# Performance work log

Measured on AMD Instinct MI355X. Metric: run time of the kernel, lower is better.

The kernel has to match this reference:

```python
import jax, jax.numpy as jnp
import numpy as np

DIM = 1024
HEADS = 16
DIM_HEAD = 64
INNER = HEADS * DIM_HEAD  # 1024
SCALE = DIM_HEAD ** -0.5


def setup_inputs() -> dict:
    key = jax.random.key(0)
    ks = jax.random.split(key, 5)
    B, N = 4, 2048
    x = jax.random.normal(ks[0], (B, N, DIM), dtype=jnp.float32)
    # torch Linear weights are [out, in]; store transposed [in, out] for x @ W
    s = 1.0 / np.sqrt(DIM)
    Wq = jax.random.uniform(ks[1], (DIM, INNER), minval=-s, maxval=s, dtype=jnp.float32)
    Wkv = jax.random.uniform(ks[2], (DIM, 2 * INNER), minval=-s, maxval=s, dtype=jnp.float32)
    so = 1.0 / np.sqrt(INNER)
    Wo = jax.random.uniform(ks[3], (INNER, DIM), minval=-so, maxval=so, dtype=jnp.float32)
    bo = jax.random.uniform(ks[4], (DIM,), minval=-so, maxval=so, dtype=jnp.float32)
    return {"x": x, "Wq": Wq, "Wkv": Wkv, "Wo": Wo, "bo": bo}


def reference(x, Wq, Wkv, Wo, bo):
    B, N, _ = x.shape
    q = x @ Wq                      # [B, N, INNER]
    kv = x @ Wkv                    # [B, N, 2*INNER]
    k, v = jnp.split(kv, 2, axis=-1)

    def split_heads(t):
        return t.reshape(B, N, HEADS, DIM_HEAD).transpose(0, 2, 1, 3)  # [B,H,N,D]

    q, k, v = split_heads(q) * SCALE, split_heads(k), split_heads(v)
    sim = jnp.einsum('bhid,bhjd->bhij', q, k)  # [B,H,N,N]
    mask_value = -jnp.finfo(sim.dtype).max
    # causal: mask strictly-upper triangle (triu with offset j-i+1 = 1)
    causal_mask = jnp.triu(jnp.ones((N, N), dtype=bool), k=1)
    sim = jnp.where(causal_mask[None, None, :, :], mask_value, sim)
    attn = jax.nn.softmax(sim, axis=-1)
    out = jnp.einsum('bhij,bhjd->bhid', attn, v)            # [B,H,N,D]
    out = out.transpose(0, 2, 1, 3).reshape(B, N, INNER)    # [B,N,INNER]
    return out @ Wo + bo
```

## Files before the change

kernel.cpp:

```cpp
#include <hip/hip_runtime.h>

typedef unsigned short u16;
typedef __bf16 bf16x8 __attribute__((ext_vector_type(8)));
typedef float floatx4 __attribute__((ext_vector_type(4)));
typedef unsigned as1_u32 __attribute__((address_space(1)));
typedef unsigned as3_u32 __attribute__((address_space(3)));

__device__ inline u16 f2bf(float f) {
    unsigned int u = __builtin_bit_cast(unsigned int, f);
    u += 0x7fffu + ((u >> 16) & 1u);
    return (u16)(u >> 16);
}
__device__ inline u16 f2bf_trunc(float f) {
    return (u16)(__builtin_bit_cast(unsigned int, f) >> 16);
}
__device__ inline floatx4 mfma16(bf16x8 a, bf16x8 b, floatx4 c) {
    return __builtin_amdgcn_mfma_f32_16x16x32_bf16(a, b, c, 0, 0, 0);
}
__device__ inline void gld16(const u16* g, u16* l) {
    __builtin_amdgcn_global_load_lds((const as1_u32*)g, (as3_u32*)l, 16, 0, 0);
}

#define NSEQ 2048
#define DIM  1024
#define HEADS 16
#define DHEAD 64
#define QSCALE 0.18033688f
#define CSHIFT 4.328085f

__global__ __launch_bounds__(256) void conv_x(const float* __restrict__ src,
                                              u16* __restrict__ dst) {
    const size_t i = ((size_t)blockIdx.x * 256 + threadIdx.x) * 8;
    float4 a = *(const float4*)&src[i];
    float4 b = *(const float4*)&src[i + 4];
    u16 o[8] __attribute__((aligned(16)));
    o[0] = f2bf(a.x); o[1] = f2bf(a.y); o[2] = f2bf(a.z); o[3] = f2bf(a.w);
    o[4] = f2bf(b.x); o[5] = f2bf(b.y); o[6] = f2bf(b.z); o[7] = f2bf(b.w);
    *(uint4*)&dst[i] = *(const uint4*)o;
}

__global__ __launch_bounds__(256) void transpose_conv(const float* __restrict__ src,
                                                      u16* __restrict__ dst, int ncols) {
    __shared__ u16 tile[64][72];
    const int n0 = blockIdx.x * 64, k0 = blockIdx.y * 64;
    const int t = threadIdx.x;
    #pragma unroll
    for (int rr = 0; rr < 4; rr++) {
        const int k = (t >> 4) + rr * 16;
        const int n = (t & 15) * 4;
        float4 v = *(const float4*)&src[(size_t)(k0 + k) * ncols + n0 + n];
        tile[n + 0][k] = f2bf(v.x); tile[n + 1][k] = f2bf(v.y);
        tile[n + 2][k] = f2bf(v.z); tile[n + 3][k] = f2bf(v.w);
    }
    __syncthreads();
    #pragma unroll
    for (int ww = 0; ww < 2; ww++) {
        const int idx = t + ww * 256;
        const int n = idx >> 3, g = idx & 7;
        u16 tmp[8] __attribute__((aligned(16)));
        #pragma unroll
        for (int i = 0; i < 8; i++) tmp[i] = tile[n][g * 8 + i];
        *(uint4*)&dst[(size_t)(n0 + n) * 1024 + k0 + g * 8] = *(const uint4*)tmp;
    }
}

__global__ __launch_bounds__(256) void qkv_gemm_v2(
    const u16* __restrict__ xb, const u16* __restrict__ Wt,
    u16* __restrict__ q_ws, u16* __restrict__ k_ws, u16* __restrict__ v_ws)
{
    __shared__ u16 a_lds[128 * 32];
    __shared__ u16 b_lds[128 * 32];

    const int n0 = blockIdx.x * 128;
    const int m0 = blockIdx.y * 128;
    const int t = threadIdx.x, lane = t & 63, w = t >> 6;
    const int wr = w >> 1, wc = w & 1;
    const int quad = lane >> 4, l16 = lane & 15;
    const int lrow = lane >> 2, lk = (lane & 3) * 8;

    floatx4 acc[4][4];
    #pragma unroll
    for (int i = 0; i < 4; i++)
        #pragma unroll
        for (int j = 0; j < 4; j++) acc[i][j] = floatx4{0.f, 0.f, 0.f, 0.f};

    for (int k0 = 0; k0 < DIM; k0 += 32) {
        __syncthreads();
        #pragma unroll
        for (int hh = 0; hh < 2; hh++) {
            const int row = w * 32 + hh * 16;
            gld16(&xb[(size_t)(m0 + row + lrow) * DIM + k0 + lk], &a_lds[row * 32]);
            gld16(&Wt[(size_t)(n0 + row + lrow) * DIM + k0 + lk], &b_lds[row * 32]);
        }
        __syncthreads();

        bf16x8 af[4], bf[4];
        #pragma unroll
        for (int i = 0; i < 4; i++)
            af[i] = *(const bf16x8*)&a_lds[(wr * 64 + i * 16 + l16) * 32 + quad * 8];
        #pragma unroll
        for (int j = 0; j < 4; j++)
            bf[j] = *(const bf16x8*)&b_lds[(wc * 64 + j * 16 + l16) * 32 + quad * 8];
        #pragma unroll
        for (int i = 0; i < 4; i++)
            #pragma unroll
            for (int j = 0; j < 4; j++)
                acc[i][j] = mfma16(af[i], bf[j], acc[i][j]);
    }

    const int seg = n0 >> 10;
    #pragma unroll
    for (int j = 0; j < 4; j++) {
        const int n  = n0 + wc * 64 + j * 16 + l16;
        const int nn = n & 1023;
        const int h  = nn >> 6, d = nn & 63;
        #pragma unroll
        for (int i = 0; i < 4; i++) {
            const int mb = m0 + wr * 64 + i * 16 + quad * 4;
            const int b = mb >> 11, ib = mb & (NSEQ - 1);
            if (seg == 0) {
                #pragma unroll
                for (int r = 0; r < 4; r++)
                    q_ws[(((size_t)(b * HEADS + h)) * NSEQ + ib + r) * DHEAD + d] =
                        f2bf(acc[i][j][r] * QSCALE);
            } else if (seg == 1) {
                #pragma unroll
                for (int r = 0; r < 4; r++)
                    k_ws[(((size_t)(b * HEADS + h)) * NSEQ + ib + r) * DHEAD + d] =
                        f2bf(acc[i][j][r]);
            } else {
                u16 tmp[4] __attribute__((aligned(8)));
                #pragma unroll
                for (int r = 0; r < 4; r++) tmp[r] = f2bf(acc[i][j][r]);
                *(uint2*)&v_ws[(((size_t)(b * HEADS + h)) * DHEAD + d) * NSEQ + ib] =
                    *(const uint2*)tmp;
            }
        }
    }
}

__global__ __launch_bounds__(256) void attn_v4(
    const u16* __restrict__ q_ws, const u16* __restrict__ k_ws,
    const u16* __restrict__ v_ws, u16* __restrict__ attn_ws)
{
    __shared__ u16 k_lds[64 * 72];
    __shared__ u16 v_lds[64 * 72];
    __shared__ u16 p_lds[4 * 32 * 72];

    const int bid = blockIdx.x;
    const int bh  = bid & 63;
    const int t16 = 15 - (bid >> 6);
    const int i0  = t16 * 128;
    const int b   = bh >> 4, h = bh & 15;

    const u16* qb = q_ws + (size_t)bh * NSEQ * DHEAD;
    const u16* kb = k_ws + (size_t)bh * NSEQ * DHEAD;
    const u16* vb = v_ws + (size_t)bh * DHEAD * NSEQ;

    const int t    = threadIdx.x;
    const int lane = t & 63, w = t >> 6;
    const int quad = lane >> 4, l16 = lane & 15;

    bf16x8 qf[2][2];
    #pragma unroll
    for (int rf = 0; rf < 2; rf++)
        #pragma unroll
        for (int dg = 0; dg < 2; dg++)
            qf[rf][dg] = *(const bf16x8*)&qb[(size_t)(i0 + rf * 64 + w * 16 + l16) * DHEAD
                                             + dg * 32 + quad * 8];

    float l_r[2][4];
    floatx4 acc[2][4];
    #pragma unroll
    for (int rf = 0; rf < 2; rf++) {
        #pragma unroll
        for (int r = 0; r < 4; r++) l_r[rf][r] = 0.f;
        #pragma unroll
        for (int dg = 0; dg < 4; dg++) acc[rf][dg] = floatx4{0.f, 0.f, 0.f, 0.f};
    }

    const int srow = t >> 2, spart = t & 3;
    const int jt_max = 2 * t16 + 1;

    for (int jt = 0; jt <= jt_max; jt++) {
        const int j0 = jt * 64;
        __syncthreads();
        *(uint4*)&k_lds[srow * 72 + spart * 16] =
            *(const uint4*)&kb[(size_t)(j0 + srow) * DHEAD + spart * 16];
        *(uint4*)&k_lds[srow * 72 + spart * 16 + 8] =
            *(const uint4*)&kb[(size_t)(j0 + srow) * DHEAD + spart * 16 + 8];
        *(uint4*)&v_lds[srow * 72 + spart * 16] =
            *(const uint4*)&vb[(size_t)srow * NSEQ + j0 + spart * 16];
        *(uint4*)&v_lds[srow * 72 + spart * 16 + 8] =
            *(const uint4*)&vb[(size_t)srow * NSEQ + j0 + spart * 16 + 8];
        __syncthreads();

        floatx4 s[2][4];
        #pragma unroll
        for (int rf = 0; rf < 2; rf++)
            #pragma unroll
            for (int g = 0; g < 4; g++) s[rf][g] = floatx4{0.f, 0.f, 0.f, 0.f};
        #pragma unroll
        for (int dg = 0; dg < 2; dg++)
            #pragma unroll
            for (int g = 0; g < 4; g++) {
                bf16x8 kf = *(const bf16x8*)&k_lds[(g * 16 + l16) * 72 + dg * 32 + quad * 8];
                s[0][g] = mfma16(qf[0][dg], kf, s[0][g]);
                s[1][g] = mfma16(qf[1][dg], kf, s[1][g]);
            }

        #pragma unroll
        for (int rf = 0; rf < 2; rf++) {
            const int imin = i0 + rf * 64 + w * 16;
            if (j0 + 63 > imin) {
                #pragma unroll
                for (int g = 0; g < 4; g++) {
                    const int j = j0 + g * 16 + l16;
                    #pragma unroll
                    for (int r = 0; r < 4; r++)
                        if (j > imin + quad * 4 + r) s[rf][g][r] = -1e30f;
                }
            }
        }

        #pragma unroll
        for (int rf = 0; rf < 2; rf++)
            #pragma unroll
            for (int g = 0; g < 4; g++)
                #pragma unroll
                for (int r = 0; r < 4; r++) {
                    const float p = __builtin_amdgcn_exp2f(s[rf][g][r] - CSHIFT);
                    s[rf][g][r] = p;
                    l_r[rf][r] += p;
                }

        #pragma unroll
        for (int rf = 0; rf < 2; rf++)
            #pragma unroll
            for (int g = 0; g < 4; g++)
                #pragma unroll
                for (int r = 0; r < 4; r++)
                    p_lds[w * 2304 + (rf * 16 + quad * 4 + r) * 72 + g * 16 + l16] =
                        f2bf_trunc(s[rf][g][r]);
        asm volatile("s_waitcnt lgkmcnt(0)" ::: "memory");

        #pragma unroll
        for (int jg = 0; jg < 2; jg++) {
            bf16x8 pf0 = *(const bf16x8*)&p_lds[w * 2304 + l16 * 72 + jg * 32 + quad * 8];
            bf16x8 pf1 = *(const bf16x8*)&p_lds[w * 2304 + (16 + l16) * 72 + jg * 32 + quad * 8];
            #pragma unroll
            for (int dg = 0; dg < 4; dg++) {
                bf16x8 vf = *(const bf16x8*)&v_lds[(dg * 16 + l16) * 72 + jg * 32 + quad * 8];
                acc[0][dg] = mfma16(pf0, vf, acc[0][dg]);
                acc[1][dg] = mfma16(pf1, vf, acc[1][dg]);
            }
        }
    }

    #pragma unroll
    for (int rf = 0; rf < 2; rf++) {
        #pragma unroll
        for (int off = 1; off < 16; off <<= 1)
            #pragma unroll
            for (int r = 0; r < 4; r++)
                l_r[rf][r] += __shfl_xor(l_r[rf][r], off);
        #pragma unroll
        for (int dg = 0; dg < 4; dg++)
            #pragma unroll
            for (int r = 0; r < 4; r++) {
                const float o = acc[rf][dg][r] / l_r[rf][r];
                const int i = i0 + rf * 64 + w * 16 + quad * 4 + r;
                attn_ws[(((size_t)(b * NSEQ + i)) * HEADS + h) * DHEAD + dg * 16 + l16] = f2bf(o);
            }
    }
}

__global__ __launch_bounds__(256) void out_gemm_v2(
    const u16* __restrict__ attn, const u16* __restrict__ Wot,
    const float* __restrict__ bo, float* __restrict__ out)
{
    __shared__ u16 a_lds[128 * 32];
    __shared__ u16 b_lds[128 * 32];

    const int n0 = blockIdx.x * 128;
    const int m0 = blockIdx.y * 128;
    const int t = threadIdx.x, lane = t & 63, w = t >> 6;
    const int wr = w >> 1, wc = w & 1;
    const int quad = lane >> 4, l16 = lane & 15;
    const int lrow = lane >> 2, lk = (lane & 3) * 8;

    floatx4 acc[4][4];
    #pragma unroll
    for (int i = 0; i < 4; i++)
        #pragma unroll
        for (int j = 0; j < 4; j++) acc[i][j] = floatx4{0.f, 0.f, 0.f, 0.f};

    for (int k0 = 0; k0 < DIM; k0 += 32) {
        __syncthreads();
        #pragma unroll
        for (int hh = 0; hh < 2; hh++) {
            const int row = w * 32 + hh * 16;
            gld16(&attn[(size_t)(m0 + row + lrow) * DIM + k0 + lk], &a_lds[row * 32]);
            gld16(&Wot[(size_t)(n0 + row + lrow) * DIM + k0 + lk], &b_lds[row * 32]);
        }
        __syncthreads();

        bf16x8 af[4], bf[4];
        #pragma unroll
        for (int i = 0; i < 4; i++)
            af[i] = *(const bf16x8*)&a_lds[(wr * 64 + i * 16 + l16) * 32 + quad * 8];
        #pragma unroll
        for (int j = 0; j < 4; j++)
            bf[j] = *(const bf16x8*)&b_lds[(wc * 64 + j * 16 + l16) * 32 + quad * 8];
        #pragma unroll
        for (int i = 0; i < 4; i++)
            #pragma unroll
            for (int j = 0; j < 4; j++)
                acc[i][j] = mfma16(af[i], bf[j], acc[i][j]);
    }

    #pragma unroll
    for (int j = 0; j < 4; j++) {
        const int n = n0 + wc * 64 + j * 16 + l16;
        const float bias = bo[n];
        #pragma unroll
        for (int i = 0; i < 4; i++) {
            #pragma unroll
            for (int r = 0; r < 4; r++) {
                const int m = m0 + wr * 64 + i * 16 + quad * 4 + r;
                out[(size_t)m * DIM + n] = acc[i][j][r] + bias;
            }
        }
    }
}

extern "C" void kernel_launch(void* const* d_in, const int* in_sizes, int n_in,
                              void* d_out, int out_size, void* d_ws, size_t ws_size,
                              hipStream_t stream) {
    const float* x   = (const float*)d_in[0];
    const float* Wq  = (const float*)d_in[1];
    const float* Wkv = (const float*)d_in[2];
    const float* Wo  = (const float*)d_in[3];
    const float* bo  = (const float*)d_in[4];

    u16* q_ws = (u16*)d_out;
    u16* xb   = (u16*)d_out + (size_t)8388608;

    u16* ws   = (u16*)d_ws;
    u16* k_ws = ws;
    u16* v_ws = ws + (size_t)8388608;
    u16* a_ws = ws + (size_t)16777216;
    u16* Wt   = a_ws;
    u16* Wot  = k_ws;

    conv_x<<<4096, 256, 0, stream>>>(x, xb);
    transpose_conv<<<dim3(16, 16), 256, 0, stream>>>(Wq, Wt, 1024);
    transpose_conv<<<dim3(32, 16), 256, 0, stream>>>(Wkv, Wt + (size_t)1024 * 1024, 2048);
    qkv_gemm_v2<<<dim3(24, 64), 256, 0, stream>>>(xb, Wt, q_ws, k_ws, v_ws);
    attn_v4<<<dim3(1024), 256, 0, stream>>>(q_ws, k_ws, v_ws, a_ws);
    transpose_conv<<<dim3(16, 16), 256, 0, stream>>>(Wo, Wot, 1024);
    out_gemm_v2<<<dim3(8, 64), 256, 0, stream>>>(a_ws, Wot, bo, (float*)d_out);
}
```

Before: 280.2 us.

## Double K-step per sync in GEMMs and transpose S tile in attention

Both GEMMs now load a 64-wide K slab per iteration into two LDS buffers, halving the barrier count per K and issuing more loads per sync. The attention kernel swaps MFMA operand order so each lane holds four consecutive keys of one query row. This lets P be written to LDS as packed 8-byte stores instead of scalar 2-byte stores, and row sums are reduced with fewer shuffles. The trade-off is doubled LDS use in the GEMMs, which may lower occupancy.

```diff
diff --git a/kernel.cpp b/kernel.cpp
--- a/kernel.cpp
+++ b/kernel.cpp
@@ -11,14 +11,18 @@
     u += 0x7fffu + ((u >> 16) & 1u);
     return (u16)(u >> 16);
 }
-__device__ inline u16 f2bf_trunc(float f) {
-    return (u16)(__builtin_bit_cast(unsigned int, f) >> 16);
-}
 __device__ inline floatx4 mfma16(bf16x8 a, bf16x8 b, floatx4 c) {
     return __builtin_amdgcn_mfma_f32_16x16x32_bf16(a, b, c, 0, 0, 0);
 }
 __device__ inline void gld16(const u16* g, u16* l) {
     __builtin_amdgcn_global_load_lds((const as1_u32*)g, (as3_u32*)l, 16, 0, 0);
+}
+__device__ inline uint2 pack4bf(float a, float b, float c, float d) {
+    unsigned ua = __builtin_bit_cast(unsigned, a) >> 16;
+    unsigned ub = __builtin_bit_cast(unsigned, b) & 0xffff0000u;
+    unsigned uc = __builtin_bit_cast(unsigned, c) >> 16;
+    unsigned ud = __builtin_bit_cast(unsigned, d) & 0xffff0000u;
+    return uint2{ua | ub, uc | ud};
 }
 
 #define NSEQ 2048
@@ -64,12 +68,12 @@
     }
 }
 
-__global__ __launch_bounds__(256) void qkv_gemm_v2(
+__global__ __launch_bounds__(256) void qkv_gemm_v3(
     const u16* __restrict__ xb, const u16* __restrict__ Wt,
     u16* __restrict__ q_ws, u16* __restrict__ k_ws, u16* __restrict__ v_ws)
 {
-    __shared__ u16 a_lds[128 * 32];
-    __shared__ u16 b_lds[128 * 32];
+    __shared__ u16 a0[128 * 32], a1[128 * 32];
+    __shared__ u16 b0[128 * 32], b1[128 * 32];
 
     const int n0 = blockIdx.x * 128;
     const int m0 = blockIdx.y * 128;
@@ -84,28 +88,37 @@
         #pragma unroll
         for (int j = 0; j < 4; j++) acc[i][j] = floatx4{0.f, 0.f, 0.f, 0.f};
 
-    for (int k0 = 0; k0 < DIM; k0 += 32) {
+    for (int k0 = 0; k0 < DIM; k0 += 64) {
         __syncthreads();
         #pragma unroll
         for (int hh = 0; hh < 2; hh++) {
             const int row = w * 32 + hh * 16;
-            gld16(&xb[(size_t)(m0 + row + lrow) * DIM + k0 + lk], &a_lds[row * 32]);
-            gld16(&Wt[(size_t)(n0 + row + lrow) * DIM + k0 + lk], &b_lds[row * 32]);
-        }
-        __syncthreads();
-
-        bf16x8 af[4], bf[4];
-        #pragma unroll
-        for (int i = 0; i < 4; i++)
-            af[i] = *(const bf16x8*)&a_lds[(wr * 64 + i * 16 + l16) * 32 + quad * 8];
-        #pragma unroll
-        for (int j = 0; j < 4; j++)
-            bf[j] = *(const bf16x8*)&b_lds[(wc * 64 + j * 16 + l16) * 32 + quad * 8];
-        #pragma unroll
-        for (int i = 0; i < 4; i++)
+            const size_t ga = (size_t)(m0 + row + lrow) * DIM + k0 + lk;
+            const size_t gb = (size_t)(n0 + row + lrow) * DIM + k0 + lk;
+            gld16(&xb[ga],      &a0[row * 32]);
+            gld16(&xb[ga + 32], &a1[row * 32]);
+            gld16(&Wt[gb],      &b0[row * 32]);
+            gld16(&Wt[gb + 32], &b1[row * 32]);
+        }
+        __syncthreads();
+
+        #pragma unroll
+        for (int ks = 0; ks < 2; ks++) {
+            const u16* al = ks ? a1 : a0;
+            const u16* bl = ks ? b1 : b0;
+            bf16x8 af[4], bf[4];
+            #pragma unroll
+            for (int i = 0; i < 4; i++)
+                af[i] = *(const bf16x8*)&al[(wr * 64 + i * 16 + l16) * 32 + quad * 8];
             #pragma unroll
             for (int j = 0; j < 4; j++)
-                acc[i][j] = mfma16(af[i], bf[j], acc[i][j]);
+                bf[j] = *(const bf16x8*)&bl[(wc * 64 + j * 16 + l16) * 32 + quad * 8];
+            #pragma unroll
+            for (int i = 0; i < 4; i++)
+                #pragma unroll
+                for (int j = 0; j < 4; j++)
+                    acc[i][j] = mfma16(af[i], bf[j], acc[i][j]);
+        }
     }
 
     const int seg = n0 >> 10;
@@ -139,7 +152,7 @@
     }
 }
 
-__global__ __launch_bounds__(256) void attn_v4(
+__global__ __launch_bounds__(256) void attn_v5(
     const u16* __restrict__ q_ws, const u16* __restrict__ k_ws,
     const u16* __restrict__ v_ws, u16* __restrict__ attn_ws)
 {
@@ -169,15 +182,12 @@
             qf[rf][dg] = *(const bf16x8*)&qb[(size_t)(i0 + rf * 64 + w * 16 + l16) * DHEAD
                                              + dg * 32 + quad * 8];
 
-    float l_r[2][4];
+    float l_ln[2] = {0.f, 0.f};
     floatx4 acc[2][4];
     #pragma unroll
-    for (int rf = 0; rf < 2; rf++) {
-        #pragma unroll
-        for (int r = 0; r < 4; r++) l_r[rf][r] = 0.f;
+    for (int rf = 0; rf < 2; rf++)
         #pragma unroll
         for (int dg = 0; dg < 4; dg++) acc[rf][dg] = floatx4{0.f, 0.f, 0.f, 0.f};
-    }
 
     const int srow = t >> 2, spart = t & 3;
     const int jt_max = 2 * t16 + 1;
@@ -205,43 +215,39 @@
             #pragma unroll
             for (int g = 0; g < 4; g++) {
                 bf16x8 kf = *(const bf16x8*)&k_lds[(g * 16 + l16) * 72 + dg * 32 + quad * 8];
-                s[0][g] = mfma16(qf[0][dg], kf, s[0][g]);
-                s[1][g] = mfma16(qf[1][dg], kf, s[1][g]);
+                s[0][g] = mfma16(kf, qf[0][dg], s[0][g]);
+                s[1][g] = mfma16(kf, qf[1][dg], s[1][g]);
             }
 
         #pragma unroll
         for (int rf = 0; rf < 2; rf++) {
             const int imin = i0 + rf * 64 + w * 16;
             if (j0 + 63 > imin) {
+                const int i = imin + l16;
                 #pragma unroll
                 for (int g = 0; g < 4; g++) {
-                    const int j = j0 + g * 16 + l16;
+                    const int jb = j0 + g * 16 + quad * 4;
                     #pragma unroll
                     for (int r = 0; r < 4; r++)
-                        if (j > imin + quad * 4 + r) s[rf][g][r] = -1e30f;
+                        if (jb + r > i) s[rf][g][r] = -1e30f;
                 }
             }
         }
 
         #pragma unroll
-        for (int rf = 0; rf < 2; rf++)
-            #pragma unroll
-            for (int g = 0; g < 4; g++)
+        for (int rf = 0; rf < 2; rf++) {
+            #pragma unroll
+            for (int g = 0; g < 4; g++) {
                 #pragma unroll
                 for (int r = 0; r < 4; r++) {
                     const float p = __builtin_amdgcn_exp2f(s[rf][g][r] - CSHIFT);
                     s[rf][g][r] = p;
-                    l_r[rf][r] += p;
+                    l_ln[rf] += p;
                 }
-
-        #pragma unroll
-        for (int rf = 0; rf < 2; rf++)
-            #pragma unroll
-            for (int g = 0; g < 4; g++)
-                #pragma unroll
-                for (int r = 0; r < 4; r++)
-                    p_lds[w * 2304 + (rf * 16 + quad * 4 + r) * 72 + g * 16 + l16] =
-                        f2bf_trunc(s[rf][g][r]);
+                *(uint2*)&p_lds[w * 2304 + (rf * 16 + l16) * 72 + g * 16 + quad * 4] =
+                    pack4bf(s[rf][g][0], s[rf][g][1], s[rf][g][2], s[rf][g][3]);
+            }
+        }
         asm volatile("s_waitcnt lgkmcnt(0)" ::: "memory");
 
         #pragma unroll
@@ -259,28 +265,33 @@
 
     #pragma unroll
     for (int rf = 0; rf < 2; rf++) {
-        #pragma unroll
-        for (int off = 1; off < 16; off <<= 1)
-            #pragma unroll
-            for (int r = 0; r < 4; r++)
-                l_r[rf][r] += __shfl_xor(l_r[rf][r], off);
+        l_ln[rf] += __shfl_xor(l_ln[rf], 16);
+        l_ln[rf] += __shfl_xor(l_ln[rf], 32);
+    }
+
+    #pragma unroll
+    for (int rf = 0; rf < 2; rf++) {
+        float l_row[4];
+        #pragma unroll
+        for (int r = 0; r < 4; r++)
+            l_row[r] = __shfl(l_ln[rf], quad * 4 + r);
         #pragma unroll
         for (int dg = 0; dg < 4; dg++)
             #pragma unroll
             for (int r = 0; r < 4; r++) {
-                const float o = acc[rf][dg][r] / l_r[rf][r];
+                const float o = acc[rf][dg][r] / l_row[r];
                 const int i = i0 + rf * 64 + w * 16 + quad * 4 + r;
                 attn_ws[(((size_t)(b * NSEQ + i)) * HEADS + h) * DHEAD + dg * 16 + l16] = f2bf(o);
             }
     }
 }
 
-__global__ __launch_bounds__(256) void out_gemm_v2(
+__global__ __launch_bounds__(256) void out_gemm_v3(
     const u16* __restrict__ attn, const u16* __restrict__ Wot,
     const float* __restrict__ bo, float* __restrict__ out)
 {
-    __shared__ u16 a_lds[128 * 32];
-    __shared__ u16 b_lds[128 * 32];
+    __shared__ u16 a0[128 * 32], a1[128 * 32];
+    __shared__ u16 b0[128 * 32], b1[128 * 32];
 
     const int n0 = blockIdx.x * 128;
     const int m0 = blockIdx.y * 128;
@@ -295,28 +306,37 @@
         #pragma unroll
         for (int j = 0; j < 4; j++) acc[i][j] = floatx4{0.f, 0.f, 0.f, 0.f};
 
-    for (int k0 = 0; k0 < DIM; k0 += 32) {
+    for (int k0 = 0; k0 < DIM; k0 += 64) {
         __syncthreads();
         #pragma unroll
         for (int hh = 0; hh < 2; hh++) {
             const int row = w * 32 + hh * 16;
-            gld16(&attn[(size_t)(m0 + row + lrow) * DIM + k0 + lk], &a_lds[row * 32]);
-            gld16(&Wot[(size_t)(n0 + row + lrow) * DIM + k0 + lk], &b_lds[row * 32]);
-        }
-        __syncthreads();
-
-        bf16x8 af[4], bf[4];
-        #pragma unroll
-        for (int i = 0; i < 4; i++)
-            af[i] = *(const bf16x8*)&a_lds[(wr * 64 + i * 16 + l16) * 32 + quad * 8];
-        #pragma unroll
-        for (int j = 0; j < 4; j++)
-            bf[j] = *(const bf16x8*)&b_lds[(wc * 64 + j * 16 + l16) * 32 + quad * 8];
-        #pragma unroll
-        for (int i = 0; i < 4; i++)
+            const size_t ga = (size_t)(m0 + row + lrow) * DIM + k0 + lk;
+            const size_t gb = (size_t)(n0 + row + lrow) * DIM + k0 + lk;
+            gld16(&attn[ga],      &a0[row * 32]);
+            gld16(&attn[ga + 32], &a1[row * 32]);
+            gld16(&Wot[gb],       &b0[row * 32]);
+            gld16(&Wot[gb + 32],  &b1[row * 32]);
+        }
+        __syncthreads();
+
+        #pragma unroll
+        for (int ks = 0; ks < 2; ks++) {
+            const u16* al = ks ? a1 : a0;
+            const u16* bl = ks ? b1 : b0;
+            bf16x8 af[4], bf[4];
+            #pragma unroll
+            for (int i = 0; i < 4; i++)
+                af[i] = *(const bf16x8*)&al[(wr * 64 + i * 16 + l16) * 32 + quad * 8];
             #pragma unroll
             for (int j = 0; j < 4; j++)
-                acc[i][j] = mfma16(af[i], bf[j], acc[i][j]);
+                bf[j] = *(const bf16x8*)&bl[(wc * 64 + j * 16 + l16) * 32 + quad * 8];
+            #pragma unroll
+            for (int i = 0; i < 4; i++)
+                #pragma unroll
+                for (int j = 0; j < 4; j++)
+                    acc[i][j] = mfma16(af[i], bf[j], acc[i][j]);
+        }
     }
 
     #pragma unroll
@@ -356,8 +376,8 @@
     conv_x<<<4096, 256, 0, stream>>>(x, xb);
     transpose_conv<<<dim3(16, 16), 256, 0, stream>>>(Wq, Wt, 1024);
     transpose_conv<<<dim3(32, 16), 256, 0, stream>>>(Wkv, Wt + (size_t)1024 * 1024, 2048);
-    qkv_gemm_v2<<<dim3(24, 64), 256, 0, stream>>>(xb, Wt, q_ws, k_ws, v_ws);
-    attn_v4<<<dim3(1024), 256, 0, stream>>>(q_ws, k_ws, v_ws, a_ws);
+    qkv_gemm_v3<<<dim3(24, 64), 256, 0, stream>>>(xb, Wt, q_ws, k_ws, v_ws);
+    attn_v5<<<dim3(1024), 256, 0, stream>>>(q_ws, k_ws, v_ws, a_ws);
     transpose_conv<<<dim3(16, 16), 256, 0, stream>>>(Wo, Wot, 1024);
-    out_gemm_v2<<<dim3(8, 64), 256, 0, stream>>>(a_ws, Wot, bo, (float*)d_out);
-}
+    out_gemm_v3<<<dim3(8, 64), 256, 0, stream>>>(a_ws, Wot, bo, (float*)d_out);
+}
```

After: 261.3 us. 1.07x faster.
